# Optimization experiments

Hardware: AMD Instinct MI355X
Metric: run time of the kernel (lower is better)

Reference implementation:

```python
import jax, jax.numpy as jnp
import numpy as np

N = 50000
E = 800000
IN_C = 128
OUT_C = 256
NUM_REL = 6


def _rgcn_conv(x, src, dst, etype, W, root, bias):
    # PyG RGCNConv (no bases, aggr='mean'):
    # out = x @ root + bias + sum_r mean_{j in N_r(i)}(x_j) @ W[r]
    n = x.shape[0]
    xe = x[src]  # [E, d_in] gather of source features
    out = x @ root + bias
    for r in range(NUM_REL):
        m = (etype == r)
        s = jax.ops.segment_sum(jnp.where(m[:, None], xe, 0.0), dst, num_segments=n)
        c = jax.ops.segment_sum(m.astype(x.dtype), dst, num_segments=n)
        out = out + (s / jnp.maximum(c, 1.0)[:, None]) @ W[r]
    return out


def setup_inputs() -> dict:
    key = jax.random.key(0)
    ks = jax.random.split(key, 16)
    half = OUT_C // 2

    def g(k, shape, fan_in):
        return jax.random.normal(k, shape, dtype=jnp.float32) / np.sqrt(fan_in)

    return {
        "x": jax.random.normal(ks[0], (N, IN_C), dtype=jnp.float32),
        "edge_index": jax.random.randint(ks[1], (2, E), 0, N, dtype=jnp.int32),
        "edge_type": jax.random.randint(ks[2], (E,), 0, NUM_REL, dtype=jnp.int32),
        # encoder MLP
        "enc_w0": g(ks[3], (IN_C, OUT_C), IN_C), "enc_b0": jnp.zeros((OUT_C,), jnp.float32),
        "enc_w1": g(ks[4], (OUT_C, OUT_C), OUT_C), "enc_b1": jnp.zeros((OUT_C,), jnp.float32),
        "enc_w2": g(ks[5], (OUT_C, half), OUT_C), "enc_b2": jnp.zeros((half,), jnp.float32),
        # conv1
        "W1": g(ks[6], (NUM_REL, IN_C, OUT_C), IN_C), "root1": g(ks[7], (IN_C, OUT_C), IN_C),
        "b1": jnp.zeros((OUT_C,), jnp.float32),
        # conv2
        "W2": g(ks[8], (NUM_REL, OUT_C, OUT_C), OUT_C), "root2": g(ks[9], (OUT_C, OUT_C), OUT_C),
        "b2": jnp.zeros((OUT_C,), jnp.float32),
        # conv_out
        "W3": g(ks[10], (NUM_REL, OUT_C, half), OUT_C), "root3": g(ks[11], (OUT_C, half), OUT_C),
        "b3": jnp.zeros((half,), jnp.float32),
    }


def reference(x, edge_index, edge_type,
              enc_w0, enc_b0, enc_w1, enc_b1, enc_w2, enc_b2,
              W1, root1, b1, W2, root2, b2, W3, root3, b3):
    src, dst = edge_index[0], edge_index[1]
    # dense encoder branch
    h = jax.nn.relu(x @ enc_w0 + enc_b0)
    h = jax.nn.relu(h @ enc_w1 + enc_b1)
    self_feat = h @ enc_w2 + enc_b2
    # RGCN branch
    g1 = jax.nn.relu(_rgcn_conv(x, src, dst, edge_type, W1, root1, b1))
    g2 = jax.nn.relu(_rgcn_conv(g1, src, dst, edge_type, W2, root2, b2))
    graph_feat = _rgcn_conv(g2, src, dst, edge_type, W3, root3, b3)
    return jnp.concatenate([self_feat, graph_feat], axis=-1)
```

## Files before the change

kernel.cpp:

```cpp
#include <hip/hip_runtime.h>

#define NN   50000
#define EE   800000
#define INC  128
#define OUTC 256
#define HALF 128
#define NREL 6
#define NCELL (NN * NREL)
#define NPAD 50048

typedef __attribute__((ext_vector_type(4))) short s16x4;
typedef __attribute__((ext_vector_type(8))) short bf16x8;
typedef __attribute__((ext_vector_type(4))) float f32x4;

__device__ __forceinline__ float b2f(short b) {
    unsigned u = ((unsigned)(unsigned short)b) << 16;
    return __uint_as_float(u);
}
__device__ __forceinline__ short f2b(float f) {
    unsigned u = __float_as_uint(f);
    unsigned r = (u + 0x7fffu + ((u >> 16) & 1u)) >> 16;
    return (short)r;
}

__device__ __forceinline__ void gload16(const void* g, void* l) {
    __builtin_amdgcn_global_load_lds(
        (const __attribute__((address_space(1))) void*)g,
        (__attribute__((address_space(3))) void*)l, 16, 0, 0);
}

__global__ __launch_bounds__(256) void count_k(const int* __restrict__ dst,
                                               const int* __restrict__ et,
                                               int* __restrict__ cnt) {
    int e = blockIdx.x * 256 + threadIdx.x;
    if (e < EE) atomicAdd(&cnt[dst[e] * NREL + et[e]], 1);
}

__global__ __launch_bounds__(256) void scanA_k(const int* __restrict__ cnt,
                                               int* __restrict__ off,
                                               int* __restrict__ bsum, int n) {
    __shared__ int sh[256];
    int t = threadIdx.x;
    int base = blockIdx.x * 512 + t * 2;
    int v0 = (base < n) ? cnt[base] : 0;
    int v1 = (base + 1 < n) ? cnt[base + 1] : 0;
    int s = v0 + v1;
    sh[t] = s; __syncthreads();
    for (int o = 1; o < 256; o <<= 1) {
        int u = (t >= o) ? sh[t - o] : 0;
        __syncthreads();
        sh[t] += u;
        __syncthreads();
    }
    int excl = sh[t] - s;
    if (base < n)     off[base]     = excl;
    if (base + 1 < n) off[base + 1] = excl + v0;
    if (t == 255) bsum[blockIdx.x] = sh[255];
}

__global__ __launch_bounds__(1024) void scanB_k(int* __restrict__ bsum, int nb) {
    __shared__ int sh[1024];
    int t = threadIdx.x;
    int s = (t < nb) ? bsum[t] : 0;
    sh[t] = s; __syncthreads();
    for (int o = 1; o < 1024; o <<= 1) {
        int u = (t >= o) ? sh[t - o] : 0;
        __syncthreads();
        sh[t] += u;
        __syncthreads();
    }
    if (t < nb) bsum[t] = sh[t] - s;
}

__global__ __launch_bounds__(256) void scanC_k(int* __restrict__ off,
                                               const int* __restrict__ bsum, int n) {
    int i = blockIdx.x * 256 + threadIdx.x;
    if (i < n) off[i] += bsum[i >> 9];
    if (i == 0) off[n] = EE;
}

__global__ __launch_bounds__(256) void copyint_k(const int* __restrict__ a,
                                                 int* __restrict__ b, int n) {
    int i = blockIdx.x * 256 + threadIdx.x;
    if (i < n) b[i] = a[i];
}

__global__ __launch_bounds__(256) void fill_k(const int* __restrict__ src,
                                              const int* __restrict__ dst,
                                              const int* __restrict__ et,
                                              int* __restrict__ cur,
                                              int* __restrict__ es) {
    int e = blockIdx.x * 256 + threadIdx.x;
    if (e < EE) {
        int key = dst[e] * NREL + et[e];
        int p = atomicAdd(&cur[key], 1);
        es[p] = src[e];
    }
}

__global__ __launch_bounds__(256) void cast_x_k(const float* __restrict__ x,
                                                short* __restrict__ xb, int n4) {
    int i = blockIdx.x * 256 + threadIdx.x;
    if (i < n4) {
        float4 v = ((const float4*)x)[i];
        s16x4 o;
        o[0] = f2b(v.x); o[1] = f2b(v.y); o[2] = f2b(v.z); o[3] = f2b(v.w);
        ((s16x4*)xb)[i] = o;
    }
}

__global__ __launch_bounds__(256) void wtcat2_k(const float* __restrict__ root,
                                                const float* __restrict__ W,
                                                int K, int D, int Ncols,
                                                short* __restrict__ BT) {
    int i = blockIdx.x * 256 + threadIdx.x;
    if (i >= Ncols * K) return;
    int n = i / K, k = i - n * K;
    float v;
    if (n < D) {
        v = root[(size_t)k * D + n];
    } else {
        int nn = n - D;
        int r = nn / D, c = nn - r * D;
        v = W[((size_t)r * K + k) * D + c];
    }
    BT[(size_t)n * K + k] = f2b(v);
}

#define ACH(R, q) ((((R) << 2) | ((q) ^ ((R) & 3) ^ (((R) >> 2) & 1))) * 8)

__global__ __launch_bounds__(256) void gemm_bt_k(
    const short* __restrict__ A, int lda,
    const short* __restrict__ BT,
    int M, int K, int Ncols,
    const float* __restrict__ bias, int relu,
    short* __restrict__ Cb, int ldcb,
    float* __restrict__ Cf, int ldcf) {
    __shared__ __align__(16) char smem[16384];
    short* As = (short*)smem;
    short* Bs = As + 128 * 32;
    const int tid = threadIdx.x;
    const int wave = tid >> 6, lane = tid & 63;
    const int wm = (wave & 1) * 64, wn = (wave >> 1) * 64;
    const int l16 = lane & 15, quad = lane >> 4;
    const int bm = blockIdx.x * 128, bn = blockIdx.y * 128;

    const int s0 = tid, s1 = tid + 256;
    const int r0 = s0 >> 2, c0 = (s0 & 3) ^ (r0 & 3) ^ ((r0 >> 2) & 1);
    const int r1 = s1 >> 2, c1 = (s1 & 3) ^ (r1 & 3) ^ ((r1 >> 2) & 1);

    f32x4 acc[4][4];
    #pragma unroll
    for (int i = 0; i < 4; ++i)
        #pragma unroll
        for (int j = 0; j < 4; ++j)
            acc[i][j] = (f32x4)0.f;

    for (int k0 = 0; k0 < K; k0 += 32) {
        gload16(A + (size_t)(bm + r0) * lda + k0 + c0 * 8, As + (wave * 64) * 8);
        gload16(A + (size_t)(bm + r1) * lda + k0 + c1 * 8, As + (256 + wave * 64) * 8);
        gload16(BT + (size_t)(bn + r0) * K + k0 + c0 * 8, Bs + (wave * 64) * 8);
        gload16(BT + (size_t)(bn + r1) * K + k0 + c1 * 8, Bs + (256 + wave * 64) * 8);
        __syncthreads();
        bf16x8 af[4], bf[4];
        #pragma unroll
        for (int mt = 0; mt < 4; ++mt)
            af[mt] = *(const bf16x8*)&As[ACH(wm + mt * 16 + l16, quad)];
        #pragma unroll
        for (int nt = 0; nt < 4; ++nt)
            bf[nt] = *(const bf16x8*)&Bs[ACH(wn + nt * 16 + l16, quad)];
        #pragma unroll
        for (int mt = 0; mt < 4; ++mt)
            #pragma unroll
            for (int nt = 0; nt < 4; ++nt)
                acc[mt][nt] = __builtin_amdgcn_mfma_f32_16x16x32_bf16(
                    af[mt], bf[nt], acc[mt][nt], 0, 0, 0);
        __syncthreads();
    }

    float bv[4];
    #pragma unroll
    for (int nt = 0; nt < 4; ++nt)
        bv[nt] = bias ? bias[bn + wn + nt * 16 + l16] : 0.f;

    if (Cb) {
        short* Es = (short*)smem;
        #pragma unroll
        for (int mt = 0; mt < 4; ++mt) {
            __syncthreads();
            int srb = (wave & 1) * 16 + quad * 4;
            #pragma unroll
            for (int nt = 0; nt < 4; ++nt) {
                int sc = wn + nt * 16 + l16;
                #pragma unroll
                for (int r = 0; r < 4; ++r) {
                    float v = acc[mt][nt][r] + bv[nt];
                    if (relu) v = fmaxf(v, 0.f);
                    Es[(srb + r) * 128 + sc] = f2b(v);
                }
            }
            __syncthreads();
            #pragma unroll
            for (int h = 0; h < 2; ++h) {
                int c = tid + h * 256;
                int rr = c >> 4, cc = c & 15;
                int grow = bm + (rr >> 4) * 64 + mt * 16 + (rr & 15);
                if (grow < M)
                    *(bf16x8*)(Cb + (size_t)grow * ldcb + bn + cc * 8) =
                        *(const bf16x8*)&Es[rr * 128 + cc * 8];
            }
        }
    } else {
        float* Ef = (float*)smem;
        #pragma unroll
        for (int mt = 0; mt < 4; ++mt) {
            __syncthreads();
            int srb = (wave & 1) * 16 + quad * 4;
            #pragma unroll
            for (int nt = 0; nt < 4; ++nt) {
                int sc = wn + nt * 16 + l16;
                #pragma unroll
                for (int r = 0; r < 4; ++r) {
                    float v = acc[mt][nt][r] + bv[nt];
                    if (relu) v = fmaxf(v, 0.f);
                    Ef[(srb + r) * 128 + sc] = v;
                }
            }
            __syncthreads();
            #pragma unroll
            for (int h = 0; h < 4; ++h) {
                int c = tid + h * 256;
                int rr = c >> 5, cc = c & 31;
                int grow = bm + (rr >> 4) * 64 + mt * 16 + (rr & 15);
                if (grow < M)
                    *(float4*)(Cf + (size_t)grow * ldcf + bn + cc * 4) =
                        *(const float4*)&Ef[rr * 128 + cc * 4];
            }
        }
    }
}

template<int D>
__global__ __launch_bounds__(256) void gagg_k(
    const short* __restrict__ H, int ldh,
    int rfirst, int rlast, int colbase, int self0,
    const int* __restrict__ off, const int* __restrict__ es,
    const float* __restrict__ accin,
    const float* __restrict__ bias, int relu,
    short* __restrict__ Ob, float* __restrict__ Of, int ldo) {
    constexpr int LPN = D / 4;
    constexpr int NPB = 256 / LPN;
    int sub = threadIdx.x / LPN, lane = threadIdx.x % LPN;
    int node = blockIdx.x * NPB + sub;
    if (node >= NN) return;
    int c0 = lane * 4;

    float a0, a1, a2, a3;
    if (accin) {
        float4 t = *(const float4*)(accin + (size_t)node * D + c0);
        a0 = t.x; a1 = t.y; a2 = t.z; a3 = t.w;
    } else {
        a0 = a1 = a2 = a3 = 0.f;
    }
    if (self0) {
        s16x4 v = *(const s16x4*)(H + (size_t)node * ldh + c0);
        a0 += b2f(v[0]); a1 += b2f(v[1]); a2 += b2f(v[2]); a3 += b2f(v[3]);
    }
    int cell0 = node * NREL;
    for (int r = rfirst; r < rlast; ++r) {
        int beg = off[cell0 + r], end = off[cell0 + r + 1];
        if (end == beg) continue;
        int colo = (colbase + r) * D + c0;
        float s0 = 0.f, s1 = 0.f, s2 = 0.f, s3 = 0.f;
        int j = beg;
        for (; j + 1 < end; j += 2) {
            s16x4 v = *(const s16x4*)(H + (size_t)es[j] * ldh + colo);
            s16x4 w = *(const s16x4*)(H + (size_t)es[j + 1] * ldh + colo);
            s0 += b2f(v[0]) + b2f(w[0]);
            s1 += b2f(v[1]) + b2f(w[1]);
            s2 += b2f(v[2]) + b2f(w[2]);
            s3 += b2f(v[3]) + b2f(w[3]);
        }
        if (j < end) {
            s16x4 v = *(const s16x4*)(H + (size_t)es[j] * ldh + colo);
            s0 += b2f(v[0]); s1 += b2f(v[1]); s2 += b2f(v[2]); s3 += b2f(v[3]);
        }
        float inv = 1.f / (float)(end - beg);
        a0 += s0 * inv; a1 += s1 * inv; a2 += s2 * inv; a3 += s3 * inv;
    }
    if (bias) {
        float4 bv = *(const float4*)(bias + c0);
        a0 += bv.x; a1 += bv.y; a2 += bv.z; a3 += bv.w;
    }
    if (relu) {
        a0 = fmaxf(a0, 0.f); a1 = fmaxf(a1, 0.f);
        a2 = fmaxf(a2, 0.f); a3 = fmaxf(a3, 0.f);
    }
    if (Ob) {
        s16x4 o;
        o[0] = f2b(a0); o[1] = f2b(a1); o[2] = f2b(a2); o[3] = f2b(a3);
        *(s16x4*)(Ob + (size_t)node * ldo + c0) = o;
    } else {
        float4 o; o.x = a0; o.y = a1; o.z = a2; o.w = a3;
        *(float4*)(Of + (size_t)node * ldo + c0) = o;
    }
}

extern "C" void kernel_launch(void* const* d_in, const int* in_sizes, int n_in,
                              void* d_out, int out_size, void* d_ws, size_t ws_size,
                              hipStream_t stream) {
    const float* x      = (const float*)d_in[0];
    const int*   ei     = (const int*)d_in[1];
    const int*   srcv   = ei;
    const int*   dstv   = ei + EE;
    const int*   et     = (const int*)d_in[2];
    const float* enc_w0 = (const float*)d_in[3];
    const float* enc_b0 = (const float*)d_in[4];
    const float* enc_w1 = (const float*)d_in[5];
    const float* enc_b1 = (const float*)d_in[6];
    const float* enc_w2 = (const float*)d_in[7];
    const float* enc_b2 = (const float*)d_in[8];
    const float* W1     = (const float*)d_in[9];
    const float* root1  = (const float*)d_in[10];
    const float* b1     = (const float*)d_in[11];
    const float* W2     = (const float*)d_in[12];
    const float* root2  = (const float*)d_in[13];
    const float* b2     = (const float*)d_in[14];
    const float* W3     = (const float*)d_in[15];
    const float* root3  = (const float*)d_in[16];
    const float* b3     = (const float*)d_in[17];
    float* out = (float*)d_out;

    char* p = (char*)d_ws;
    auto alloc = [&](size_t bytes) -> char* {
        char* r = p; p += (bytes + 255) & ~(size_t)255; return r;
    };
    short* xb  = (short*)alloc((size_t)NPAD * INC * 2);
    short* g1  = (short*)alloc((size_t)NPAD * OUTC * 2);
    short* g2  = (short*)alloc((size_t)NPAD * OUTC * 2);
    short* BT1 = (short*)alloc((size_t)1792 * INC * 2);
    short* BT2 = (short*)alloc((size_t)1792 * OUTC * 2);
    short* BT3 = (short*)alloc((size_t)896 * OUTC * 2);
    short* ET0 = (short*)alloc((size_t)OUTC * INC * 2);
    short* ET1 = (short*)alloc((size_t)OUTC * OUTC * 2);
    short* ET2 = (short*)alloc((size_t)HALF * OUTC * 2);
    int* CNT  = (int*)alloc((size_t)NCELL * 4);
    int* OFF  = (int*)alloc((size_t)(NCELL + 1) * 4);
    int* CUR  = (int*)alloc((size_t)NCELL * 4);
    int* ES   = (int*)alloc((size_t)EE * 4);
    int* BSUM = (int*)alloc(1024 * 4);
    size_t fixed = (size_t)(p - (char*)d_ws);

    bool fullH = fixed + (size_t)NPAD * 1792 * 2 <= ws_size;
    short* H = (short*)alloc(fullH ? (size_t)NPAD * 1792 * 2
                                   : (size_t)NPAD * 1024 * 2);
    float* ACC = fullH ? nullptr : (float*)alloc((size_t)NPAD * OUTC * 4);

    hipMemsetAsync(CNT, 0, (size_t)NCELL * 4, stream);
    count_k<<<EE / 256, 256, 0, stream>>>(dstv, et, CNT);
    int nbA = (NCELL + 511) / 512;
    scanA_k<<<nbA, 256, 0, stream>>>(CNT, OFF, BSUM, NCELL);
    scanB_k<<<1, 1024, 0, stream>>>(BSUM, nbA);
    scanC_k<<<(NCELL + 255) / 256, 256, 0, stream>>>(OFF, BSUM, NCELL);
    copyint_k<<<(NCELL + 255) / 256, 256, 0, stream>>>(OFF, CUR, NCELL);
    fill_k<<<EE / 256, 256, 0, stream>>>(srcv, dstv, et, CUR, ES);

    cast_x_k<<<(NN * INC / 4 + 255) / 256, 256, 0, stream>>>(x, xb, NN * INC / 4);
    auto wt = [&](const float* root, const float* W, int K, int D, int Ncols, short* BT) {
        wtcat2_k<<<(Ncols * K + 255) / 256, 256, 0, stream>>>(root, W, K, D, Ncols, BT);
    };
    wt(root1, W1, INC, OUTC, 1792, BT1);
    wt(root2, W2, OUTC, OUTC, 1792, BT2);
    wt(root3, W3, OUTC, HALF, 896, BT3);
    wt(enc_w0, nullptr, INC, OUTC, OUTC, ET0);
    wt(enc_w1, nullptr, OUTC, OUTC, OUTC, ET1);
    wt(enc_w2, nullptr, OUTC, HALF, HALF, ET2);

    auto gemm = [&](const short* A, int lda, const short* BT, int M, int K, int Ncols,
                    const float* bias, int relu, short* Cb, int ldcb, float* Cf, int ldcf) {
        dim3 grid((M + 127) / 128, Ncols / 128);
        gemm_bt_k<<<grid, 256, 0, stream>>>(A, lda, BT, M, K, Ncols,
                                            bias, relu, Cb, ldcb, Cf, ldcf);
    };

    gemm(xb, INC, ET0, NN, INC, OUTC, enc_b0, 1, g1, OUTC, nullptr, 0);
    gemm(g1, OUTC, ET1, NN, OUTC, OUTC, enc_b1, 1, g2, OUTC, nullptr, 0);
    gemm(g2, OUTC, ET2, NN, OUTC, HALF, enc_b2, 0, nullptr, 0, out, OUTC);

    auto conv = [&](const short* A, int K, int D, const short* BT,
                    const float* bias, int relu, short* Ob, float* Of) {
        int NPB = 256 / (D / 4);
        int gg = (NN + NPB - 1) / NPB;
        if (fullH) {
            gemm(A, K, BT, NN, K, 7 * D, nullptr, 0, H, 7 * D, nullptr, 0);
            if (D == 256)
                gagg_k<256><<<gg, 256, 0, stream>>>(H, 7 * D, 0, NREL, 1, 1,
                    OFF, ES, nullptr, bias, relu, Ob, Of, OUTC);
            else
                gagg_k<128><<<gg, 256, 0, stream>>>(H, 7 * D, 0, NREL, 1, 1,
                    OFF, ES, nullptr, bias, relu, Ob, Of, OUTC);
        } else {
            gemm(A, K, BT, NN, K, 4 * D, nullptr, 0, H, 4 * D, nullptr, 0);
            if (D == 256)
                gagg_k<256><<<gg, 256, 0, stream>>>(H, 4 * D, 0, 3, 1, 1,
                    OFF, ES, nullptr, nullptr, 0, nullptr, ACC, D);
            else
                gagg_k<128><<<gg, 256, 0, stream>>>(H, 4 * D, 0, 3, 1, 1,
                    OFF, ES, nullptr, nullptr, 0, nullptr, ACC, D);
            gemm(A, K, BT + (size_t)4 * D * K, NN, K, 3 * D, nullptr, 0, H, 3 * D, nullptr, 0);
            if (D == 256)
                gagg_k<256><<<gg, 256, 0, stream>>>(H, 3 * D, 3, NREL, -3, 0,
                    OFF, ES, ACC, bias, relu, Ob, Of, OUTC);
            else
                gagg_k<128><<<gg, 256, 0, stream>>>(H, 3 * D, 3, NREL, -3, 0,
                    OFF, ES, ACC, bias, relu, Ob, Of, OUTC);
        }
    };

    conv(xb, INC,  OUTC, BT1, b1, 1, g1, nullptr);
    conv(g1, OUTC, OUTC, BT2, b2, 1, g2, nullptr);
    conv(g2, OUTC, HALF, BT3, b3, 0, nullptr, out + HALF);
}
```

Measured before the change: 733.2 us.

## Co-launch encoder GEMMs with RGCN conv GEMMs in one grid

```diff
diff --git a/kernel.cpp b/kernel.cpp
--- a/kernel.cpp
+++ b/kernel.cpp
@@ -129,13 +129,14 @@
 
 #define ACH(R, q) ((((R) << 2) | ((q) ^ ((R) & 3) ^ (((R) >> 2) & 1))) * 8)
 
-__global__ __launch_bounds__(256) void gemm_bt_k(
-    const short* __restrict__ A, int lda,
-    const short* __restrict__ BT,
-    int M, int K, int Ncols,
-    const float* __restrict__ bias, int relu,
-    short* __restrict__ Cb, int ldcb,
-    float* __restrict__ Cf, int ldcf) {
+__global__ __launch_bounds__(256) void gemm2_k(
+    const short* __restrict__ A1, const short* __restrict__ B1,
+    const float* __restrict__ bias1, int relu1,
+    short* __restrict__ Cb1, int ldcb1, float* __restrict__ Cf1, int ldcf1,
+    const short* __restrict__ A2, const short* __restrict__ B2,
+    const float* __restrict__ bias2, int relu2,
+    short* __restrict__ Cb2, int ldcb2, float* __restrict__ Cf2, int ldcf2,
+    int M, int K, int nby1) {
     __shared__ __align__(16) char smem[16384];
     short* As = (short*)smem;
     short* Bs = As + 128 * 32;
@@ -143,7 +144,19 @@
     const int wave = tid >> 6, lane = tid & 63;
     const int wm = (wave & 1) * 64, wn = (wave >> 1) * 64;
     const int l16 = lane & 15, quad = lane >> 4;
-    const int bm = blockIdx.x * 128, bn = blockIdx.y * 128;
+    const int bm = blockIdx.x * 128;
+
+    const short* A; const short* BT; const float* bias;
+    int relu; short* Cb; int ldcb; float* Cf; int ldcf; int bn;
+    if ((int)blockIdx.y < nby1) {
+        A = A1; BT = B1; bias = bias1; relu = relu1;
+        Cb = Cb1; ldcb = ldcb1; Cf = Cf1; ldcf = ldcf1;
+        bn = blockIdx.y * 128;
+    } else {
+        A = A2; BT = B2; bias = bias2; relu = relu2;
+        Cb = Cb2; ldcb = ldcb2; Cf = Cf2; ldcf = ldcf2;
+        bn = (blockIdx.y - nby1) * 128;
+    }
 
     const int s0 = tid, s1 = tid + 256;
     const int r0 = s0 >> 2, c0 = (s0 & 3) ^ (r0 & 3) ^ ((r0 >> 2) & 1);
@@ -157,8 +170,8 @@
             acc[i][j] = (f32x4)0.f;
 
     for (int k0 = 0; k0 < K; k0 += 32) {
-        gload16(A + (size_t)(bm + r0) * lda + k0 + c0 * 8, As + (wave * 64) * 8);
-        gload16(A + (size_t)(bm + r1) * lda + k0 + c1 * 8, As + (256 + wave * 64) * 8);
+        gload16(A + (size_t)(bm + r0) * K + k0 + c0 * 8, As + (wave * 64) * 8);
+        gload16(A + (size_t)(bm + r1) * K + k0 + c1 * 8, As + (256 + wave * 64) * 8);
         gload16(BT + (size_t)(bn + r0) * K + k0 + c0 * 8, Bs + (wave * 64) * 8);
         gload16(BT + (size_t)(bn + r1) * K + k0 + c1 * 8, Bs + (256 + wave * 64) * 8);
         __syncthreads();
@@ -273,15 +286,17 @@
         int colo = (colbase + r) * D + c0;
         float s0 = 0.f, s1 = 0.f, s2 = 0.f, s3 = 0.f;
         int j = beg;
-        for (; j + 1 < end; j += 2) {
-            s16x4 v = *(const s16x4*)(H + (size_t)es[j] * ldh + colo);
-            s16x4 w = *(const s16x4*)(H + (size_t)es[j + 1] * ldh + colo);
-            s0 += b2f(v[0]) + b2f(w[0]);
-            s1 += b2f(v[1]) + b2f(w[1]);
-            s2 += b2f(v[2]) + b2f(w[2]);
-            s3 += b2f(v[3]) + b2f(w[3]);
+        for (; j + 3 < end; j += 4) {
+            s16x4 v0 = *(const s16x4*)(H + (size_t)es[j] * ldh + colo);
+            s16x4 v1 = *(const s16x4*)(H + (size_t)es[j + 1] * ldh + colo);
+            s16x4 v2 = *(const s16x4*)(H + (size_t)es[j + 2] * ldh + colo);
+            s16x4 v3 = *(const s16x4*)(H + (size_t)es[j + 3] * ldh + colo);
+            s0 += b2f(v0[0]) + b2f(v1[0]) + b2f(v2[0]) + b2f(v3[0]);
+            s1 += b2f(v0[1]) + b2f(v1[1]) + b2f(v2[1]) + b2f(v3[1]);
+            s2 += b2f(v0[2]) + b2f(v1[2]) + b2f(v2[2]) + b2f(v3[2]);
+            s3 += b2f(v0[3]) + b2f(v1[3]) + b2f(v2[3]) + b2f(v3[3]);
         }
-        if (j < end) {
+        for (; j < end; ++j) {
             s16x4 v = *(const s16x4*)(H + (size_t)es[j] * ldh + colo);
             s0 += b2f(v[0]); s1 += b2f(v[1]); s2 += b2f(v[2]); s3 += b2f(v[3]);
         }
@@ -351,10 +366,14 @@
     int* BSUM = (int*)alloc(1024 * 4);
     size_t fixed = (size_t)(p - (char*)d_ws);
 
-    bool fullH = fixed + (size_t)NPAD * 1792 * 2 <= ws_size;
-    short* H = (short*)alloc(fullH ? (size_t)NPAD * 1792 * 2
-                                   : (size_t)NPAD * 1024 * 2);
-    float* ACC = fullH ? nullptr : (float*)alloc((size_t)NPAD * OUTC * 4);
+    const size_t Hfull = (size_t)NPAD * 1792 * 2;
+    const size_t Esz   = (size_t)NPAD * OUTC * 2;
+    bool tierA = fixed + Hfull + 2 * Esz + 1024 <= ws_size;
+    bool fullH = tierA || (fixed + Hfull + 1024 <= ws_size);
+    short* H = (short*)alloc(fullH ? Hfull : (size_t)NPAD * 1024 * 2);
+    short* e1 = nullptr; short* e2 = nullptr; float* ACC = nullptr;
+    if (tierA) { e1 = (short*)alloc(Esz); e2 = (short*)alloc(Esz); }
+    if (!fullH) ACC = (float*)alloc((size_t)NPAD * OUTC * 4);
 
     hipMemsetAsync(CNT, 0, (size_t)NCELL * 4, stream);
     count_k<<<EE / 256, 256, 0, stream>>>(dstv, et, CNT);
@@ -376,23 +395,46 @@
     wt(enc_w1, nullptr, OUTC, OUTC, OUTC, ET1);
     wt(enc_w2, nullptr, OUTC, HALF, HALF, ET2);
 
-    auto gemm = [&](const short* A, int lda, const short* BT, int M, int K, int Ncols,
-                    const float* bias, int relu, short* Cb, int ldcb, float* Cf, int ldcf) {
+    auto gemm1 = [&](const short* A, const short* BT, int M, int K, int Ncols,
+                     const float* bias, int relu, short* Cb, int ldcb, float* Cf, int ldcf) {
         dim3 grid((M + 127) / 128, Ncols / 128);
-        gemm_bt_k<<<grid, 256, 0, stream>>>(A, lda, BT, M, K, Ncols,
-                                            bias, relu, Cb, ldcb, Cf, ldcf);
+        gemm2_k<<<grid, 256, 0, stream>>>(A, BT, bias, relu, Cb, ldcb, Cf, ldcf,
+                                          A, BT, bias, relu, Cb, ldcb, Cf, ldcf,
+                                          M, K, grid.y);
     };
 
-    gemm(xb, INC, ET0, NN, INC, OUTC, enc_b0, 1, g1, OUTC, nullptr, 0);
-    gemm(g1, OUTC, ET1, NN, OUTC, OUTC, enc_b1, 1, g2, OUTC, nullptr, 0);
-    gemm(g2, OUTC, ET2, NN, OUTC, HALF, enc_b2, 0, nullptr, 0, out, OUTC);
+    if (tierA) {
+        gemm2_k<<<dim3(391, 16), 256, 0, stream>>>(
+            xb, BT1, nullptr, 0, H, 1792, nullptr, 0,
+            xb, ET0, enc_b0, 1, e1, OUTC, nullptr, 0,
+            NN, INC, 14);
+        gagg_k<256><<<12500, 256, 0, stream>>>(H, 1792, 0, NREL, 1, 1,
+            OFF, ES, nullptr, b1, 1, g1, nullptr, OUTC);
+        gemm2_k<<<dim3(391, 16), 256, 0, stream>>>(
+            g1, BT2, nullptr, 0, H, 1792, nullptr, 0,
+            e1, ET1, enc_b1, 1, e2, OUTC, nullptr, 0,
+            NN, OUTC, 14);
+        gagg_k<256><<<12500, 256, 0, stream>>>(H, 1792, 0, NREL, 1, 1,
+            OFF, ES, nullptr, b2, 1, g2, nullptr, OUTC);
+        gemm2_k<<<dim3(391, 8), 256, 0, stream>>>(
+            g2, BT3, nullptr, 0, H, 896, nullptr, 0,
+            e2, ET2, enc_b2, 0, nullptr, 0, out, OUTC,
+            NN, OUTC, 7);
+        gagg_k<128><<<6250, 256, 0, stream>>>(H, 896, 0, NREL, 1, 1,
+            OFF, ES, nullptr, b3, 0, nullptr, out + HALF, OUTC);
+        return;
+    }
+
+    gemm1(xb, ET0, NN, INC, OUTC, enc_b0, 1, g1, OUTC, nullptr, 0);
+    gemm1(g1, ET1, NN, OUTC, OUTC, enc_b1, 1, g2, OUTC, nullptr, 0);
+    gemm1(g2, ET2, NN, OUTC, HALF, enc_b2, 0, nullptr, 0, out, OUTC);
 
     auto conv = [&](const short* A, int K, int D, const short* BT,
                     const float* bias, int relu, short* Ob, float* Of) {
         int NPB = 256 / (D / 4);
         int gg = (NN + NPB - 1) / NPB;
         if (fullH) {
-            gemm(A, K, BT, NN, K, 7 * D, nullptr, 0, H, 7 * D, nullptr, 0);
+            gemm1(A, BT, NN, K, 7 * D, nullptr, 0, H, 7 * D, nullptr, 0);
             if (D == 256)
                 gagg_k<256><<<gg, 256, 0, stream>>>(H, 7 * D, 0, NREL, 1, 1,
                     OFF, ES, nullptr, bias, relu, Ob, Of, OUTC);
@@ -400,14 +442,14 @@
                 gagg_k<128><<<gg, 256, 0, stream>>>(H, 7 * D, 0, NREL, 1, 1,
                     OFF, ES, nullptr, bias, relu, Ob, Of, OUTC);
         } else {
-            gemm(A, K, BT, NN, K, 4 * D, nullptr, 0, H, 4 * D, nullptr, 0);
+            gemm1(A, BT, NN, K, 4 * D, nullptr, 0, H, 4 * D, nullptr, 0);
             if (D == 256)
                 gagg_k<256><<<gg, 256, 0, stream>>>(H, 4 * D, 0, 3, 1, 1,
                     OFF, ES, nullptr, nullptr, 0, nullptr, ACC, D);
             else
                 gagg_k<128><<<gg, 256, 0, stream>>>(H, 4 * D, 0, 3, 1, 1,
                     OFF, ES, nullptr, nullptr, 0, nullptr, ACC, D);
-            gemm(A, K, BT + (size_t)4 * D * K, NN, K, 3 * D, nullptr, 0, H, 3 * D, nullptr, 0);
+            gemm1(A, BT + (size_t)4 * D * (size_t)K, NN, K, 3 * D, nullptr, 0, H, 3 * D, nullptr, 0);
             if (D == 256)
                 gagg_k<256><<<gg, 256, 0, stream>>>(H, 3 * D, 3, NREL, -3, 0,
                     OFF, ES, ACC, bias, relu, Ob, Of, OUTC);
```

Result: no change. 740.9 us (+1.1%).
